# Performance work log

Hardware: AMD Instinct MI355X
Metric: run time of the kernel (lower is better)

## Reference

```python
import jax, jax.numpy as jnp
import numpy as np

B, N, FIN, H, L = 64, 512, 1024, 128, 512
K1, K2, K3 = 256, 128, 64  # top-k pooling keeps half the nodes each stage
CO = 32  # 4 conv branches (k=3,5,7,9) x 32 channels = 128 text-CNN features


def _gcn(A, X, W, b):
    deg = A.sum(-1)
    d = jnp.where(deg > 0, jax.lax.rsqrt(deg), 0.0)
    h = (X @ W) * d[..., None]          # project first (FIN -> H reduces work)
    h = jnp.einsum('bnm,bmh->bnh', A, h)
    return h * d[..., None] + b


def _pool(A, X, p, k):
    # Lupool ~ TopKPooling: learned projection score, keep top-k nodes, gate features
    score = jnp.tanh((X @ p) / (jnp.linalg.norm(p) + 1e-12))  # [B, n]
    _, idx = jax.lax.top_k(score, k)                          # [B, k]
    Xs = jnp.take_along_axis(X, idx[..., None], axis=1)
    Xs = Xs * jnp.take_along_axis(score, idx, axis=1)[..., None]
    As = jax.vmap(lambda a, i: a[i][:, i])(A, idx)            # induced subgraph
    return As, Xs


def _readout(X):
    # DGL AvgPooling / MaxPooling over nodes, concatenated -> [B, 2H]
    return jnp.concatenate([X.mean(axis=1), X.max(axis=1)], axis=1)


def _conv_branch(x_ncl, w, b):
    y = jax.lax.conv_general_dilated(x_ncl, w, (1,), 'VALID',
                                     dimension_numbers=('NCH', 'OIH', 'NCH'))
    return jax.nn.relu(y + b[None, :, None]).max(axis=2)  # global max over time


def setup_inputs():
    key = jax.random.key(0)
    ks = jax.random.split(key, 20)
    u = jax.random.uniform(ks[0], (B, N, N))
    A = (u < 0.01).astype(jnp.float32)
    A = jnp.maximum(A, jnp.swapaxes(A, 1, 2))
    A = A.at[:, jnp.arange(N), jnp.arange(N)].set(1.0)

    def pr(i, shape):
        return jax.random.normal(ks[i], shape, jnp.float32) * 0.05

    return {
        'adj': A,
        'feat': jax.random.normal(ks[1], (B, N, FIN), jnp.float32),
        'pad_dmap': jax.random.normal(ks[2], (B, L, FIN), jnp.float32),
        'W1': pr(3, (FIN, H)), 'b1': jnp.zeros((H,), jnp.float32), 'p1': pr(4, (H,)),
        'W2': pr(5, (H, H)), 'b2': jnp.zeros((H,), jnp.float32), 'p2': pr(6, (H,)),
        'W3': pr(7, (H, H)), 'b3': jnp.zeros((H,), jnp.float32), 'p3': pr(8, (H,)),
        'cat_w': pr(9, (2 * H, H)), 'cat_b': jnp.zeros((H,), jnp.float32),
        'cw0': pr(10, (CO, FIN, 3)), 'cb0': jnp.zeros((CO,), jnp.float32),
        'cw1': pr(11, (CO, FIN, 5)), 'cb1': jnp.zeros((CO,), jnp.float32),
        'cw2': pr(12, (CO, FIN, 7)), 'cb2': jnp.zeros((CO,), jnp.float32),
        'cw3': pr(13, (CO, FIN, 9)), 'cb3': jnp.zeros((CO,), jnp.float32),
        'tf_w': pr(14, (4 * CO, H)), 'tf_b': jnp.zeros((H,), jnp.float32),
        'w1_gate': jnp.array(0.5, jnp.float32),
        'fc1_w': pr(15, (H, 512)), 'fc1_b': jnp.zeros((512,), jnp.float32),
        'fc2_w': pr(16, (512, 256)), 'fc2_b': jnp.zeros((256,), jnp.float32),
        'out_w': pr(17, (256, 2)), 'out_b': jnp.zeros((2,), jnp.float32),
    }


def reference(adj, feat, pad_dmap, W1, b1, p1, W2, b2, p2, W3, b3, p3,
              cat_w, cat_b, cw0, cb0, cw1, cb1, cw2, cb2, cw3, cb3,
              tf_w, tf_b, w1_gate, fc1_w, fc1_b, fc2_w, fc2_b, out_w, out_b):
    # --- 3-stage GraphConv + Lupool with readouts ---
    g1 = jax.nn.relu(_gcn(adj, feat, W1, b1))
    A1, x1 = _pool(adj, g1, p1, K1)
    r1 = _readout(x1)
    g2 = jax.nn.relu(_gcn(A1, x1, W2, b2))
    A2, x2 = _pool(A1, g2, p2, K2)
    r2 = _readout(x2)
    g3 = jax.nn.relu(_gcn(A2, x2, W3, b3))
    A3, x3 = _pool(A2, g3, p3, K3)
    r3 = _readout(x3)
    readout = r1 + r2 + r3                       # [B, 256]
    gnn = jax.nn.relu(readout @ cat_w + cat_b)   # [B, 128]
    # --- text-CNN branch ---
    xt = jnp.swapaxes(pad_dmap, 1, 2)            # [B, FIN, L]
    seq = jnp.concatenate([
        _conv_branch(xt, cw0, cb0), _conv_branch(xt, cw1, cb1),
        _conv_branch(xt, cw2, cb2), _conv_branch(xt, cw3, cb3)], axis=1)  # [B,128]
    seq1 = jax.nn.relu(seq @ tf_w + tf_b)
    # --- gated fusion + MLP head (dropout = identity at inference) ---
    w = jax.nn.sigmoid(w1_gate)
    gc = (1.0 - w) * gnn + w * seq1
    gc = jax.nn.relu(gc @ fc1_w + fc1_b)
    gc = jax.nn.relu(gc @ fc2_w + fc2_b)
    out = jax.nn.relu(gc @ out_w + out_b)
    return jax.nn.softmax(out, axis=1)
```

## Files before the change

kernel.cpp:

```cpp
#include <hip/hip_runtime.h>
#include <math.h>

#define B64  64
#define NN   512
#define FINN 1024
#define HH   128
#define LL   512
#define KK1  256
#define KK2  128
#define KK3  64

typedef __attribute__((ext_vector_type(8))) short short8v;
typedef __attribute__((ext_vector_type(4))) short short4v;
typedef __attribute__((ext_vector_type(4))) float f32x4;

__device__ __forceinline__ float wsum(float v) {
#pragma unroll
    for (int off = 32; off; off >>= 1) v += __shfl_xor(v, off, 64);
    return v;
}

__device__ __forceinline__ short f2bf(float x) {
    union { float f; unsigned u; } v; v.f = x;
    unsigned r = v.u + 0x7fffu + ((v.u >> 16) & 1u);
    return (short)(r >> 16);
}

#define LDAP 40
__global__ __launch_bounds__(256) void mfma_gemm(
    const float* __restrict__ A, const short* __restrict__ BT,
    float* __restrict__ C, int M, int N, int K,
    const float* __restrict__ rowscale, int ntx, int swz)
{
    __shared__ short As[128 * LDAP];
    __shared__ short Bs[128 * LDAP];
    int bid = blockIdx.x;
    if (swz) bid = (bid & 7) * (gridDim.x >> 3) + (bid >> 3);
    const int m0 = (bid / ntx) * 128;
    const int n0 = (bid % ntx) * 128;
    const int tid = threadIdx.x;
    const int lane = tid & 63;
    const int wid = tid >> 6;
    const int wr = (wid >> 1) * 64;
    const int wc = (wid & 1) * 64;

    f32x4 acc[4][4];
#pragma unroll
    for (int i = 0; i < 4; ++i)
#pragma unroll
        for (int j = 0; j < 4; ++j) acc[i][j] = (f32x4){0.f, 0.f, 0.f, 0.f};

    const int srow = tid >> 1;
    const int skq = (tid & 1) * 16;
    const float* Aptr = A + (size_t)(m0 + srow) * K + skq;
    const short* Bptr = BT + (size_t)(n0 + srow) * K + skq;

    const int fr = lane & 15;
    const int fk = (lane >> 4) * 8;
    const int crow = (lane >> 4) * 4;

    for (int k0 = 0; k0 < K; k0 += 32) {
        float4 fa0 = *(const float4*)(Aptr + k0);
        float4 fa1 = *(const float4*)(Aptr + k0 + 4);
        float4 fa2 = *(const float4*)(Aptr + k0 + 8);
        float4 fa3 = *(const float4*)(Aptr + k0 + 12);
        float4 fb0 = *(const float4*)(Bptr + k0);
        float4 fb1 = *(const float4*)(Bptr + k0 + 8);
        __syncthreads();
        short8v ha, hb;
        ha[0] = f2bf(fa0.x); ha[1] = f2bf(fa0.y); ha[2] = f2bf(fa0.z); ha[3] = f2bf(fa0.w);
        ha[4] = f2bf(fa1.x); ha[5] = f2bf(fa1.y); ha[6] = f2bf(fa1.z); ha[7] = f2bf(fa1.w);
        hb[0] = f2bf(fa2.x); hb[1] = f2bf(fa2.y); hb[2] = f2bf(fa2.z); hb[3] = f2bf(fa2.w);
        hb[4] = f2bf(fa3.x); hb[5] = f2bf(fa3.y); hb[6] = f2bf(fa3.z); hb[7] = f2bf(fa3.w);
        *(short8v*)&As[srow * LDAP + skq] = ha;
        *(short8v*)&As[srow * LDAP + skq + 8] = hb;
        *(short8v*)&Bs[srow * LDAP + skq] = *(const short8v*)&fb0;
        *(short8v*)&Bs[srow * LDAP + skq + 8] = *(const short8v*)&fb1;
        __syncthreads();

        short8v af[4], bfr[4];
#pragma unroll
        for (int i = 0; i < 4; ++i) {
            af[i] = *(const short8v*)&As[(wr + i * 16 + fr) * LDAP + fk];
            bfr[i] = *(const short8v*)&Bs[(wc + i * 16 + fr) * LDAP + fk];
        }
#pragma unroll
        for (int mi = 0; mi < 4; ++mi)
#pragma unroll
            for (int ni = 0; ni < 4; ++ni)
                acc[mi][ni] = __builtin_amdgcn_mfma_f32_16x16x32_bf16(
                    af[mi], bfr[ni], acc[mi][ni], 0, 0, 0);
    }

#pragma unroll
    for (int mi = 0; mi < 4; ++mi) {
#pragma unroll
        for (int ni = 0; ni < 4; ++ni) {
            int col = n0 + wc + ni * 16 + fr;
#pragma unroll
            for (int r = 0; r < 4; ++r) {
                int row = m0 + wr + mi * 16 + crow + r;
                float v = acc[mi][ni][r];
                if (rowscale) v *= rowscale[row];
                C[(size_t)row * N + col] = v;
            }
        }
    }
}

__global__ __launch_bounds__(256) void prep_kernel(
    const float* __restrict__ adj, float* __restrict__ dinv,
    const float* __restrict__ cw0, const float* __restrict__ cw1,
    const float* __restrict__ cw2, const float* __restrict__ cw3,
    short* __restrict__ WT,
    const float* __restrict__ W1, short* __restrict__ W1T,
    const float* __restrict__ W2, short* __restrict__ W2T,
    const float* __restrict__ W3, short* __restrict__ W3T,
    const float* __restrict__ p1, const float* __restrict__ p2,
    const float* __restrict__ p3, float* __restrict__ pnorm)
{
    const int bid = blockIdx.x, tid = threadIdx.x;
    if (bid < 8192) {
        int wid = (bid * 256 + tid) >> 6;
        int lane = tid & 63;
        const float* Arow = adj + (size_t)wid * NN;
        float s = 0.f;
        for (int c = lane; c < NN; c += 64) s += Arow[c];
        s = wsum(s);
        if (lane == 0) dinv[wid] = (s > 0.f) ? rsqrtf(s) : 0.f;
    } else if (bid < 8960) {
        int e = (bid - 8192) * 1024 + tid * 4;
        int col = e >> 10, ci = e & 1023;
        const float* cw; int k, base;
        if (col < 96)       { cw = cw0; k = 3; base = 0; }
        else if (col < 256) { cw = cw1; k = 5; base = 96; }
        else if (col < 480) { cw = cw2; k = 7; base = 256; }
        else                { cw = cw3; k = 9; base = 480; }
        int rel = col - base;
        int j = rel >> 5, co = rel & 31;
        short4v o;
#pragma unroll
        for (int q = 0; q < 4; ++q)
            o[q] = f2bf(cw[((size_t)co * FINN + ci + q) * k + j]);
        *(short4v*)&WT[e] = o;
    } else if (bid < 9088) {
        int e = (bid - 8960) * 1024 + tid * 4;
        int n = e >> 10, kq = e & 1023;
        short4v o;
#pragma unroll
        for (int q = 0; q < 4; ++q) o[q] = f2bf(W1[(size_t)(kq + q) * HH + n]);
        *(short4v*)&W1T[e] = o;
    } else if (bid < 9104) {
        int e = (bid - 9088) * 1024 + tid * 4;
        int n = e >> 7, kq = e & 127;
        short4v o;
#pragma unroll
        for (int q = 0; q < 4; ++q) o[q] = f2bf(W2[(size_t)(kq + q) * HH + n]);
        *(short4v*)&W2T[e] = o;
    } else if (bid < 9120) {
        int e = (bid - 9104) * 1024 + tid * 4;
        int n = e >> 7, kq = e & 127;
        short4v o;
#pragma unroll
        for (int q = 0; q < 4; ++q) o[q] = f2bf(W3[(size_t)(kq + q) * HH + n]);
        *(short4v*)&W3T[e] = o;
    } else {
        int w = tid >> 6, lane = tid & 63;
        if (w < 3) {
            const float* p = (w == 0) ? p1 : (w == 1) ? p2 : p3;
            float v0 = p[lane], v1 = p[lane + 64];
            float s = wsum(v0 * v0 + v1 * v1);
            if (lane == 0) pnorm[w] = sqrtf(s);
        }
    }
}

__global__ __launch_bounds__(256) void spmm_gcn(
    const float* __restrict__ A, const float* __restrict__ Hin,
    const float* __restrict__ dinv, const float* __restrict__ bias,
    const float* __restrict__ p, const float* __restrict__ pnorm,
    float* __restrict__ Gout, float* __restrict__ score, int n)
{
    int wid = (blockIdx.x * blockDim.x + threadIdx.x) >> 6;
    int lane = threadIdx.x & 63;
    int b = wid / n, row = wid % n;
    const float* Arow = A + ((size_t)b * n + row) * n;
    float acc0 = 0.f, acc1 = 0.f;
    for (int c = 0; c < n; c += 64) {
        float av = Arow[c + lane];
        unsigned long long mask = __ballot(av != 0.0f);
        while (mask) {
            int i = __ffsll((unsigned long long)mask) - 1;
            mask &= mask - 1;
            float val = __shfl(av, i, 64);
            const float* hr = Hin + ((size_t)b * n + c + i) * HH;
            acc0 = fmaf(val, hr[lane], acc0);
            acc1 = fmaf(val, hr[lane + 64], acc1);
        }
    }
    float dv = dinv[b * n + row];
    float g0 = fmaxf(fmaf(acc0, dv, bias[lane]), 0.f);
    float g1 = fmaxf(fmaf(acc1, dv, bias[lane + 64]), 0.f);
    float* gr = Gout + ((size_t)b * n + row) * HH;
    gr[lane] = g0;
    gr[lane + 64] = g1;
    float s = g0 * p[lane] + g1 * p[lane + 64];
    s = wsum(s);
    if (lane == 0) score[b * n + row] = tanhf(s / (pnorm[0] + 1e-12f));
}

__global__ __launch_bounds__(256) void topk_kernel(
    const float* __restrict__ score, int* __restrict__ idx_out, int n, int k)
{
    __shared__ float sv[512];
    __shared__ int si[512];
    int b = blockIdx.x, tid = threadIdx.x;
    for (int j = tid; j < n; j += blockDim.x) { sv[j] = score[b * n + j]; si[j] = j; }
    __syncthreads();
    for (int sz = 2; sz <= n; sz <<= 1) {
        for (int st = sz >> 1; st; st >>= 1) {
            for (int t = tid; t < (n >> 1); t += blockDim.x) {
                int i = ((t / st) * (st << 1)) + (t % st);
                int j = i + st;
                float vi = sv[i], vj = sv[j];
                int ii = si[i], ij = si[j];
                bool descend = ((i & sz) == 0);
                bool igreater = (vi > vj) || (vi == vj && ii < ij);
                if (igreater != descend) {
                    sv[i] = vj; sv[j] = vi;
                    si[i] = ij; si[j] = ii;
                }
            }
            __syncthreads();
        }
    }
    for (int j = tid; j < k; j += blockDim.x) idx_out[b * k + j] = si[j];
}

__global__ __launch_bounds__(256) void gatherA_kernel(
    const float* __restrict__ Ain, const int* __restrict__ idx,
    float* __restrict__ Aout, float* __restrict__ dinv_out, int n, int k)
{
    int wid = (blockIdx.x * blockDim.x + threadIdx.x) >> 6;
    int lane = threadIdx.x & 63;
    int b = wid / k, i = wid % k;
    int isrc = idx[b * k + i];
    const float* src = Ain + ((size_t)b * n + isrc) * n;
    float s = 0.f;
    for (int c = lane; c < k; c += 64) {
        int jsrc = idx[b * k + c];
        float v = src[jsrc];
        Aout[((size_t)b * k + i) * k + c] = v;
        s += v;
    }
    s = wsum(s);
    if (lane == 0) dinv_out[b * k + i] = rsqrtf(s);
}

__global__ __launch_bounds__(256) void pool_finish(
    const float* __restrict__ G, const float* __restrict__ score,
    const int* __restrict__ idx, float* __restrict__ X, float* __restrict__ R,
    int n, int k, int first, int writex)
{
    __shared__ int lidx[256];
    __shared__ float lsc[256];
    __shared__ float ps[2][128], pm[2][128];
    int b = blockIdx.x, tid = threadIdx.x;
    for (int i = tid; i < k; i += 256) {
        int ii = idx[b * k + i];
        lidx[i] = ii;
        lsc[i] = score[b * n + ii];
    }
    __syncthreads();
    int h = tid & 127, half = tid >> 7;
    int i0 = half * (k >> 1), i1 = i0 + (k >> 1);
    float s = 0.f, m = -INFINITY;
    for (int i = i0; i < i1; ++i) {
        float v = G[((size_t)b * n + lidx[i]) * HH + h] * lsc[i];
        if (writex) X[((size_t)b * k + i) * HH + h] = v;
        s += v;
        m = fmaxf(m, v);
    }
    ps[half][h] = s;
    pm[half][h] = m;
    __syncthreads();
    if (tid < 128) {
        float st = ps[0][h] + ps[1][h];
        float mt = fmaxf(pm[0][h], pm[1][h]);
        float mean = st / (float)k;
        if (first) {
            R[b * 256 + h] = mean;
            R[b * 256 + 128 + h] = mt;
        } else {
            R[b * 256 + h] += mean;
            R[b * 256 + 128 + h] += mt;
        }
    }
}

__global__ __launch_bounds__(256) void conv_reduce(
    const float* __restrict__ P,
    const float* __restrict__ cb0, const float* __restrict__ cb1,
    const float* __restrict__ cb2, const float* __restrict__ cb3,
    float* __restrict__ seq)
{
    int bid = blockIdx.x;
    int chunk = bid & 7, br = (bid >> 3) & 3, b = bid >> 5;
    int k = 3 + 2 * br;
    int base = (br == 0) ? 0 : (br == 1) ? 96 : (br == 2) ? 256 : 480;
    int T = LL - k + 1;
    int co = threadIdx.x & 31, ts = threadIdx.x >> 5;
    const float* cb = (br == 0) ? cb0 : (br == 1) ? cb1 : (br == 2) ? cb2 : cb3;
    float bias = cb[co];
    int c0 = chunk * 64;
    int cend = (c0 + 64 < T) ? c0 + 64 : T;
    float m = -INFINITY;
    for (int t = c0 + ts; t < cend; t += 8) {
        float acc = 0.f;
        for (int j = 0; j < k; ++j)
            acc += P[((size_t)b * LL + t + j) * 768 + base + j * 32 + co];
        m = fmaxf(m, acc + bias);
    }
    __shared__ float red[256];
    red[threadIdx.x] = m;
    __syncthreads();
    if (threadIdx.x < 32) {
        for (int s = 1; s < 8; ++s) m = fmaxf(m, red[co + s * 32]);
        atomicMax((int*)&seq[b * 128 + br * 32 + co], __float_as_int(fmaxf(m, 0.f)));
    }
}

__global__ __launch_bounds__(256) void head_fused(
    const float* __restrict__ seq, const float* __restrict__ tf_w,
    const float* __restrict__ tf_b,
    const float* __restrict__ R, const float* __restrict__ cat_w,
    const float* __restrict__ cat_b,
    const float* __restrict__ w1_gate,
    const float* __restrict__ fc1_w, const float* __restrict__ fc1_b,
    const float* __restrict__ fc2_w, const float* __restrict__ fc2_b,
    const float* __restrict__ out_w, const float* __restrict__ out_b,
    float* __restrict__ out)
{
    int b = blockIdx.x, tid = threadIdx.x;
    __shared__ float sq[128], rr[256], g0[128], g1[512], g2[256];
    rr[tid] = R[b * 256 + tid];
    if (tid < 128) sq[tid] = seq[b * 128 + tid];
    __syncthreads();
    if (tid < 128) {
        float a = tf_b[tid];
        for (int i = 0; i < 128; ++i) a = fmaf(sq[i], tf_w[i * 128 + tid], a);
        float s1 = fmaxf(a, 0.f);
        float c = cat_b[tid];
        for (int i = 0; i < 256; ++i) c = fmaf(rr[i], cat_w[i * 128 + tid], c);
        float gn = fmaxf(c, 0.f);
        float w = 1.f / (1.f + expf(-w1_gate[0]));
        g0[tid] = (1.f - w) * gn + w * s1;
    }
    __syncthreads();
    for (int o = tid; o < 512; o += 256) {
        float a = fc1_b[o];
        for (int i = 0; i < 128; ++i) a = fmaf(g0[i], fc1_w[i * 512 + o], a);
        g1[o] = fmaxf(a, 0.f);
    }
    __syncthreads();
    {
        int o = tid;
        float a = fc2_b[o];
        for (int i = 0; i < 512; ++i) a = fmaf(g1[i], fc2_w[i * 256 + o], a);
        g2[o] = fmaxf(a, 0.f);
    }
    __syncthreads();
    if (tid < 64) {
        float a0 = 0.f, a1 = 0.f;
        for (int q = tid; q < 256; q += 64) {
            a0 = fmaf(g2[q], out_w[q * 2 + 0], a0);
            a1 = fmaf(g2[q], out_w[q * 2 + 1], a1);
        }
        a0 = wsum(a0);
        a1 = wsum(a1);
        if (tid == 0) {
            float l0 = fmaxf(a0 + out_b[0], 0.f);
            float l1 = fmaxf(a1 + out_b[1], 0.f);
            float mm = fmaxf(l0, l1);
            float e0 = expf(l0 - mm), e1 = expf(l1 - mm);
            float d = e0 + e1;
            out[b * 2 + 0] = e0 / d;
            out[b * 2 + 1] = e1 / d;
        }
    }
}

extern "C" void kernel_launch(void* const* d_in, const int* in_sizes, int n_in,
                              void* d_out, int out_size, void* d_ws, size_t ws_size,
                              hipStream_t stream)
{
    const float* adj      = (const float*)d_in[0];
    const float* feat     = (const float*)d_in[1];
    const float* pad_dmap = (const float*)d_in[2];
    const float* W1 = (const float*)d_in[3];
    const float* b1 = (const float*)d_in[4];
    const float* p1 = (const float*)d_in[5];
    const float* W2 = (const float*)d_in[6];
    const float* b2 = (const float*)d_in[7];
    const float* p2 = (const float*)d_in[8];
    const float* W3 = (const float*)d_in[9];
    const float* b3 = (const float*)d_in[10];
    const float* p3 = (const float*)d_in[11];
    const float* cat_w = (const float*)d_in[12];
    const float* cat_b = (const float*)d_in[13];
    const float* cw0 = (const float*)d_in[14];
    const float* cb0 = (const float*)d_in[15];
    const float* cw1 = (const float*)d_in[16];
    const float* cb1 = (const float*)d_in[17];
    const float* cw2 = (const float*)d_in[18];
    const float* cb2 = (const float*)d_in[19];
    const float* cw3 = (const float*)d_in[20];
    const float* cb3 = (const float*)d_in[21];
    const float* tf_w = (const float*)d_in[22];
    const float* tf_b = (const float*)d_in[23];
    const float* w1_gate = (const float*)d_in[24];
    const float* fc1_w = (const float*)d_in[25];
    const float* fc1_b = (const float*)d_in[26];
    const float* fc2_w = (const float*)d_in[27];
    const float* fc2_b = (const float*)d_in[28];
    const float* out_w = (const float*)d_in[29];
    const float* out_b = (const float*)d_in[30];
    float* out = (float*)d_out;

    char* ws = (char*)d_ws;
    auto al = [](size_t x) { return (x + 255) & ~(size_t)255; };
    size_t off = 0;
    auto alloc = [&](size_t nbytes) { size_t o = off; off += al(nbytes); return o; };

    float* pnorm  = (float*)(ws + alloc(3 * 4));
    float* dinv1  = (float*)(ws + alloc((size_t)B64 * NN * 4));
    float* score1 = (float*)(ws + alloc((size_t)B64 * NN * 4));
    int*   idx1   = (int*)  (ws + alloc((size_t)B64 * KK1 * 4));
    float* dinv2  = (float*)(ws + alloc((size_t)B64 * KK1 * 4));
    float* score2 = (float*)(ws + alloc((size_t)B64 * KK1 * 4));
    int*   idx2   = (int*)  (ws + alloc((size_t)B64 * KK2 * 4));
    float* dinv3  = (float*)(ws + alloc((size_t)B64 * KK2 * 4));
    float* score3 = (float*)(ws + alloc((size_t)B64 * KK2 * 4));
    int*   idx3   = (int*)  (ws + alloc((size_t)B64 * KK3 * 4));
    float* R      = (float*)(ws + alloc((size_t)B64 * 256 * 4));
    float* seq    = (float*)(ws + alloc((size_t)B64 * 128 * 4));
    short* W1T    = (short*)(ws + alloc((size_t)HH * FINN * 2));
    short* W2T    = (short*)(ws + alloc((size_t)HH * HH * 2));
    short* W3T    = (short*)(ws + alloc((size_t)HH * HH * 2));

    size_t big = off;
    short* WT = (short*)(ws + big);
    size_t cnnoff = big + al((size_t)768 * FINN * 2);
    float* P = (float*)(ws + cnnoff);
    size_t cnn_end = cnnoff + al((size_t)B64 * LL * 768 * 4);
    size_t g = big;
    float* HT = (float*)(ws + g); g += al((size_t)B64 * NN * HH * 4);
    float* G  = (float*)(ws + g); g += al((size_t)B64 * NN * HH * 4);
    float* A1 = (float*)(ws + g); g += al((size_t)B64 * KK1 * KK1 * 4);
    float* X1 = (float*)(ws + g); g += al((size_t)B64 * KK1 * HH * 4);
    float* A2 = (float*)(ws + g); g += al((size_t)B64 * KK2 * KK2 * 4);
    float* X2 = (float*)(ws + g); g += al((size_t)B64 * KK2 * HH * 4);
    size_t gnn_end = g;
    size_t need = (cnn_end > gnn_end) ? cnn_end : gnn_end;
    if (ws_size < need) return;

    hipMemsetAsync(seq, 0, (size_t)B64 * 128 * 4, stream);

    prep_kernel<<<9121, 256, 0, stream>>>(adj, dinv1, cw0, cw1, cw2, cw3, WT,
                                          W1, W1T, W2, W2T, W3, W3T,
                                          p1, p2, p3, pnorm);

    mfma_gemm<<<1536, 256, 0, stream>>>(pad_dmap, WT, P, B64 * LL, 768, FINN,
                                        nullptr, 6, 1);
    conv_reduce<<<2048, 256, 0, stream>>>(P, cb0, cb1, cb2, cb3, seq);

    mfma_gemm<<<256, 256, 0, stream>>>(feat, W1T, HT, B64 * NN, HH, FINN,
                                       dinv1, 1, 0);
    spmm_gcn<<<(B64 * NN) / 4, 256, 0, stream>>>(adj, HT, dinv1, b1, p1, pnorm + 0,
                                                 G, score1, NN);
    topk_kernel<<<B64, 256, 0, stream>>>(score1, idx1, NN, KK1);
    gatherA_kernel<<<(B64 * KK1) / 4, 256, 0, stream>>>(adj, idx1, A1, dinv2, NN, KK1);
    pool_finish<<<B64, 256, 0, stream>>>(G, score1, idx1, X1, R, NN, KK1, 1, 1);

    mfma_gemm<<<128, 256, 0, stream>>>(X1, W2T, HT, B64 * KK1, HH, HH,
                                       dinv2, 1, 0);
    spmm_gcn<<<(B64 * KK1) / 4, 256, 0, stream>>>(A1, HT, dinv2, b2, p2, pnorm + 1,
                                                  G, score2, KK1);
    topk_kernel<<<B64, 256, 0, stream>>>(score2, idx2, KK1, KK2);
    gatherA_kernel<<<(B64 * KK2) / 4, 256, 0, stream>>>(A1, idx2, A2, dinv3, KK1, KK2);
    pool_finish<<<B64, 256, 0, stream>>>(G, score2, idx2, X2, R, KK1, KK2, 0, 1);

    mfma_gemm<<<64, 256, 0, stream>>>(X2, W3T, HT, B64 * KK2, HH, HH,
                                      dinv3, 1, 0);
    spmm_gcn<<<(B64 * KK2) / 4, 256, 0, stream>>>(A2, HT, dinv3, b3, p3, pnorm + 2,
                                                  G, score3, KK2);
    topk_kernel<<<B64, 256, 0, stream>>>(score3, idx3, KK2, KK3);
    pool_finish<<<B64, 256, 0, stream>>>(G, score3, idx3, nullptr, R, KK2, KK3, 0, 0);

    head_fused<<<B64, 256, 0, stream>>>(seq, tf_w, tf_b, R, cat_w, cat_b, w1_gate,
                                        fc1_w, fc1_b, fc2_w, fc2_b, out_w, out_b,
                                        out);
}
```

Measured before the change: 802.8 us.

## Replace sparse ballot SpMM with dense transposed MFMA GEMMs and fuse score/topk/pool

Computes each GCN stage as two bf16 MFMA GEMMs in a transposed feature-major layout. The first projects features into a bf16 intermediate scaled by dinv. The second multiplies that intermediate by the dense adjacency, using A's symmetry, with a fused dinv/bias/ReLU epilogue. The wave-per-row ballot-based sparse SpMM is removed, trading irregular gathers for dense tensor-core work over a roughly 1%-dense adjacency. Score computation, top-k sort and pooling readout are merged into one per-batch kernel, which drops two launches per stage. This adds bf16 rounding of the intermediate and adjacency, and the score loop reads the transposed G with strided access.

```diff
diff --git a/kernel.cpp b/kernel.cpp
--- a/kernel.cpp
+++ b/kernel.cpp
@@ -27,6 +27,7 @@
 }
 
 #define LDAP 40
+
 __global__ __launch_bounds__(256) void mfma_gemm(
     const float* __restrict__ A, const short* __restrict__ BT,
     float* __restrict__ C, int M, int N, int K,
@@ -103,6 +104,92 @@
                 float v = acc[mi][ni][r];
                 if (rowscale) v *= rowscale[row];
                 C[(size_t)row * N + col] = v;
+            }
+        }
+    }
+}
+
+template <int EPI>
+__global__ __launch_bounds__(256) void tgemm(
+    const short* __restrict__ A, const float* __restrict__ Bt,
+    void* __restrict__ Cout, int K, int npb, int a_per_batch,
+    const float* __restrict__ dinv, const float* __restrict__ bias)
+{
+    __shared__ short As[128 * LDAP];
+    __shared__ short Bs[128 * LDAP];
+    const int n0 = blockIdx.x * 128;
+    const int b = n0 / npb;
+    const int nloc = n0 - b * npb;
+    const int tid = threadIdx.x;
+    const int lane = tid & 63;
+    const int wid = tid >> 6;
+    const int wr = (wid >> 1) * 64;
+    const int wc = (wid & 1) * 64;
+
+    f32x4 acc[4][4];
+#pragma unroll
+    for (int i = 0; i < 4; ++i)
+#pragma unroll
+        for (int j = 0; j < 4; ++j) acc[i][j] = (f32x4){0.f, 0.f, 0.f, 0.f};
+
+    const int srow = tid >> 1;
+    const int skq = (tid & 1) * 16;
+    const short* Aptr = A + (size_t)((a_per_batch ? b * 128 : 0) + srow) * K + skq;
+    const float* Bptr = Bt + (size_t)(n0 + srow) * K + skq;
+
+    const int fr = lane & 15;
+    const int fk = (lane >> 4) * 8;
+    const int crow = (lane >> 4) * 4;
+
+    for (int k0 = 0; k0 < K; k0 += 32) {
+        short8v a0 = *(const short8v*)(Aptr + k0);
+        short8v a1 = *(const short8v*)(Aptr + k0 + 8);
+        float4 fb0 = *(const float4*)(Bptr + k0);
+        float4 fb1 = *(const float4*)(Bptr + k0 + 4);
+        float4 fb2 = *(const float4*)(Bptr + k0 + 8);
+        float4 fb3 = *(const float4*)(Bptr + k0 + 12);
+        __syncthreads();
+        short8v hb0, hb1;
+        hb0[0] = f2bf(fb0.x); hb0[1] = f2bf(fb0.y); hb0[2] = f2bf(fb0.z); hb0[3] = f2bf(fb0.w);
+        hb0[4] = f2bf(fb1.x); hb0[5] = f2bf(fb1.y); hb0[6] = f2bf(fb1.z); hb0[7] = f2bf(fb1.w);
+        hb1[0] = f2bf(fb2.x); hb1[1] = f2bf(fb2.y); hb1[2] = f2bf(fb2.z); hb1[3] = f2bf(fb2.w);
+        hb1[4] = f2bf(fb3.x); hb1[5] = f2bf(fb3.y); hb1[6] = f2bf(fb3.z); hb1[7] = f2bf(fb3.w);
+        *(short8v*)&As[srow * LDAP + skq] = a0;
+        *(short8v*)&As[srow * LDAP + skq + 8] = a1;
+        *(short8v*)&Bs[srow * LDAP + skq] = hb0;
+        *(short8v*)&Bs[srow * LDAP + skq + 8] = hb1;
+        __syncthreads();
+
+        short8v af[4], bfr[4];
+#pragma unroll
+        for (int i = 0; i < 4; ++i) {
+            af[i] = *(const short8v*)&As[(wr + i * 16 + fr) * LDAP + fk];
+            bfr[i] = *(const short8v*)&Bs[(wc + i * 16 + fr) * LDAP + fk];
+        }
+#pragma unroll
+        for (int mi = 0; mi < 4; ++mi)
+#pragma unroll
+            for (int ni = 0; ni < 4; ++ni)
+                acc[mi][ni] = __builtin_amdgcn_mfma_f32_16x16x32_bf16(
+                    af[mi], bfr[ni], acc[mi][ni], 0, 0, 0);
+    }
+
+#pragma unroll
+    for (int mi = 0; mi < 4; ++mi) {
+#pragma unroll
+        for (int ni = 0; ni < 4; ++ni) {
+            int node_t = wc + ni * 16 + fr;
+            float dv = dinv[n0 + node_t];
+#pragma unroll
+            for (int r = 0; r < 4; ++r) {
+                int f = wr + mi * 16 + crow + r;
+                size_t oidx = ((size_t)(b * 128 + f)) * npb + nloc + node_t;
+                float v = acc[mi][ni][r] * dv;
+                if constexpr (EPI == 0) {
+                    ((short*)Cout)[oidx] = f2bf(v);
+                } else {
+                    ((float*)Cout)[oidx] = fmaxf(v + bias[f], 0.f);
+                }
             }
         }
     }
@@ -175,51 +262,32 @@
     }
 }
 
-__global__ __launch_bounds__(256) void spmm_gcn(
-    const float* __restrict__ A, const float* __restrict__ Hin,
-    const float* __restrict__ dinv, const float* __restrict__ bias,
-    const float* __restrict__ p, const float* __restrict__ pnorm,
-    float* __restrict__ Gout, float* __restrict__ score, int n)
-{
-    int wid = (blockIdx.x * blockDim.x + threadIdx.x) >> 6;
-    int lane = threadIdx.x & 63;
-    int b = wid / n, row = wid % n;
-    const float* Arow = A + ((size_t)b * n + row) * n;
-    float acc0 = 0.f, acc1 = 0.f;
-    for (int c = 0; c < n; c += 64) {
-        float av = Arow[c + lane];
-        unsigned long long mask = __ballot(av != 0.0f);
-        while (mask) {
-            int i = __ffsll((unsigned long long)mask) - 1;
-            mask &= mask - 1;
-            float val = __shfl(av, i, 64);
-            const float* hr = Hin + ((size_t)b * n + c + i) * HH;
-            acc0 = fmaf(val, hr[lane], acc0);
-            acc1 = fmaf(val, hr[lane + 64], acc1);
-        }
-    }
-    float dv = dinv[b * n + row];
-    float g0 = fmaxf(fmaf(acc0, dv, bias[lane]), 0.f);
-    float g1 = fmaxf(fmaf(acc1, dv, bias[lane + 64]), 0.f);
-    float* gr = Gout + ((size_t)b * n + row) * HH;
-    gr[lane] = g0;
-    gr[lane + 64] = g1;
-    float s = g0 * p[lane] + g1 * p[lane + 64];
-    s = wsum(s);
-    if (lane == 0) score[b * n + row] = tanhf(s / (pnorm[0] + 1e-12f));
-}
-
-__global__ __launch_bounds__(256) void topk_kernel(
-    const float* __restrict__ score, int* __restrict__ idx_out, int n, int k)
+__global__ __launch_bounds__(256) void score_topk_pool(
+    const float* __restrict__ Gt, const float* __restrict__ p,
+    const float* __restrict__ pnorm, int* __restrict__ idx_out,
+    float* __restrict__ X, float* __restrict__ R,
+    int npb, int k, int first, int writex)
 {
     __shared__ float sv[512];
     __shared__ int si[512];
+    __shared__ float pp[128];
+    __shared__ float ps[2][128], pm[2][128];
     int b = blockIdx.x, tid = threadIdx.x;
-    for (int j = tid; j < n; j += blockDim.x) { sv[j] = score[b * n + j]; si[j] = j; }
-    __syncthreads();
-    for (int sz = 2; sz <= n; sz <<= 1) {
+    if (tid < 128) pp[tid] = p[tid];
+    __syncthreads();
+    const float* Gb = Gt + (size_t)b * 128 * npb;
+    float pn = pnorm[0] + 1e-12f;
+    for (int j = tid; j < npb; j += 256) {
+        float s = 0.f;
+#pragma unroll 4
+        for (int f = 0; f < 128; ++f) s = fmaf(Gb[(size_t)f * npb + j], pp[f], s);
+        sv[j] = tanhf(s / pn);
+        si[j] = j;
+    }
+    __syncthreads();
+    for (int sz = 2; sz <= npb; sz <<= 1) {
         for (int st = sz >> 1; st; st >>= 1) {
-            for (int t = tid; t < (n >> 1); t += blockDim.x) {
+            for (int t = tid; t < (npb >> 1); t += 256) {
                 int i = ((t / st) * (st << 1)) + (t % st);
                 int j = i + st;
                 float vi = sv[i], vj = sv[j];
@@ -234,7 +302,30 @@
             __syncthreads();
         }
     }
-    for (int j = tid; j < k; j += blockDim.x) idx_out[b * k + j] = si[j];
+    for (int j = tid; j < k; j += 256) idx_out[b * k + j] = si[j];
+    int f = tid & 127, iset = tid >> 7;
+    float s = 0.f, m = -INFINITY;
+    for (int i = iset; i < k; i += 2) {
+        float v = Gb[(size_t)f * npb + si[i]] * sv[i];
+        if (writex) X[((size_t)b * k + i) * HH + f] = v;
+        s += v;
+        m = fmaxf(m, v);
+    }
+    ps[iset][f] = s;
+    pm[iset][f] = m;
+    __syncthreads();
+    if (tid < 128) {
+        float st = ps[0][f] + ps[1][f];
+        float mt = fmaxf(pm[0][f], pm[1][f]);
+        float mean = st / (float)k;
+        if (first) {
+            R[b * 256 + f] = mean;
+            R[b * 256 + 128 + f] = mt;
+        } else {
+            R[b * 256 + f] += mean;
+            R[b * 256 + 128 + f] += mt;
+        }
+    }
 }
 
 __global__ __launch_bounds__(256) void gatherA_kernel(
@@ -255,47 +346,6 @@
     }
     s = wsum(s);
     if (lane == 0) dinv_out[b * k + i] = rsqrtf(s);
-}
-
-__global__ __launch_bounds__(256) void pool_finish(
-    const float* __restrict__ G, const float* __restrict__ score,
-    const int* __restrict__ idx, float* __restrict__ X, float* __restrict__ R,
-    int n, int k, int first, int writex)
-{
-    __shared__ int lidx[256];
-    __shared__ float lsc[256];
-    __shared__ float ps[2][128], pm[2][128];
-    int b = blockIdx.x, tid = threadIdx.x;
-    for (int i = tid; i < k; i += 256) {
-        int ii = idx[b * k + i];
-        lidx[i] = ii;
-        lsc[i] = score[b * n + ii];
-    }
-    __syncthreads();
-    int h = tid & 127, half = tid >> 7;
-    int i0 = half * (k >> 1), i1 = i0 + (k >> 1);
-    float s = 0.f, m = -INFINITY;
-    for (int i = i0; i < i1; ++i) {
-        float v = G[((size_t)b * n + lidx[i]) * HH + h] * lsc[i];
-        if (writex) X[((size_t)b * k + i) * HH + h] = v;
-        s += v;
-        m = fmaxf(m, v);
-    }
-    ps[half][h] = s;
-    pm[half][h] = m;
-    __syncthreads();
-    if (tid < 128) {
-        float st = ps[0][h] + ps[1][h];
-        float mt = fmaxf(pm[0][h], pm[1][h]);
-        float mean = st / (float)k;
-        if (first) {
-            R[b * 256 + h] = mean;
-            R[b * 256 + 128 + h] = mt;
-        } else {
-            R[b * 256 + h] += mean;
-            R[b * 256 + 128 + h] += mt;
-        }
-    }
 }
 
 __global__ __launch_bounds__(256) void conv_reduce(
@@ -434,13 +484,10 @@
 
     float* pnorm  = (float*)(ws + alloc(3 * 4));
     float* dinv1  = (float*)(ws + alloc((size_t)B64 * NN * 4));
-    float* score1 = (float*)(ws + alloc((size_t)B64 * NN * 4));
+    float* dinv2  = (float*)(ws + alloc((size_t)B64 * KK1 * 4));
+    float* dinv3  = (float*)(ws + alloc((size_t)B64 * KK2 * 4));
     int*   idx1   = (int*)  (ws + alloc((size_t)B64 * KK1 * 4));
-    float* dinv2  = (float*)(ws + alloc((size_t)B64 * KK1 * 4));
-    float* score2 = (float*)(ws + alloc((size_t)B64 * KK1 * 4));
     int*   idx2   = (int*)  (ws + alloc((size_t)B64 * KK2 * 4));
-    float* dinv3  = (float*)(ws + alloc((size_t)B64 * KK2 * 4));
-    float* score3 = (float*)(ws + alloc((size_t)B64 * KK2 * 4));
     int*   idx3   = (int*)  (ws + alloc((size_t)B64 * KK3 * 4));
     float* R      = (float*)(ws + alloc((size_t)B64 * 256 * 4));
     float* seq    = (float*)(ws + alloc((size_t)B64 * 128 * 4));
@@ -454,12 +501,16 @@
     float* P = (float*)(ws + cnnoff);
     size_t cnn_end = cnnoff + al((size_t)B64 * LL * 768 * 4);
     size_t g = big;
-    float* HT = (float*)(ws + g); g += al((size_t)B64 * NN * HH * 4);
-    float* G  = (float*)(ws + g); g += al((size_t)B64 * NN * HH * 4);
-    float* A1 = (float*)(ws + g); g += al((size_t)B64 * KK1 * KK1 * 4);
-    float* X1 = (float*)(ws + g); g += al((size_t)B64 * KK1 * HH * 4);
-    float* A2 = (float*)(ws + g); g += al((size_t)B64 * KK2 * KK2 * 4);
-    float* X2 = (float*)(ws + g); g += al((size_t)B64 * KK2 * HH * 4);
+    short* Ht1 = (short*)(ws + g); g += al((size_t)B64 * HH * NN * 2);
+    float* Gt1 = (float*)(ws + g); g += al((size_t)B64 * HH * NN * 4);
+    float* A1  = (float*)(ws + g); g += al((size_t)B64 * KK1 * KK1 * 4);
+    float* X1  = (float*)(ws + g); g += al((size_t)B64 * KK1 * HH * 4);
+    short* Ht2 = (short*)(ws + g); g += al((size_t)B64 * HH * KK1 * 2);
+    float* Gt2 = (float*)(ws + g); g += al((size_t)B64 * HH * KK1 * 4);
+    float* A2  = (float*)(ws + g); g += al((size_t)B64 * KK2 * KK2 * 4);
+    float* X2  = (float*)(ws + g); g += al((size_t)B64 * KK2 * HH * 4);
+    short* Ht3 = (short*)(ws + g); g += al((size_t)B64 * HH * KK2 * 2);
+    float* Gt3 = (float*)(ws + g); g += al((size_t)B64 * HH * KK2 * 4);
     size_t gnn_end = g;
     size_t need = (cnn_end > gnn_end) ? cnn_end : gnn_end;
     if (ws_size < need) return;
@@ -474,28 +525,22 @@
                                         nullptr, 6, 1);
     conv_reduce<<<2048, 256, 0, stream>>>(P, cb0, cb1, cb2, cb3, seq);
 
-    mfma_gemm<<<256, 256, 0, stream>>>(feat, W1T, HT, B64 * NN, HH, FINN,
-                                       dinv1, 1, 0);
-    spmm_gcn<<<(B64 * NN) / 4, 256, 0, stream>>>(adj, HT, dinv1, b1, p1, pnorm + 0,
-                                                 G, score1, NN);
-    topk_kernel<<<B64, 256, 0, stream>>>(score1, idx1, NN, KK1);
+    tgemm<0><<<256, 256, 0, stream>>>(W1T, feat, Ht1, FINN, NN, 0, dinv1, nullptr);
+    tgemm<1><<<256, 256, 0, stream>>>(Ht1, adj, Gt1, NN, NN, 1, dinv1, b1);
+    score_topk_pool<<<B64, 256, 0, stream>>>(Gt1, p1, pnorm + 0, idx1, X1, R,
+                                             NN, KK1, 1, 1);
     gatherA_kernel<<<(B64 * KK1) / 4, 256, 0, stream>>>(adj, idx1, A1, dinv2, NN, KK1);
-    pool_finish<<<B64, 256, 0, stream>>>(G, score1, idx1, X1, R, NN, KK1, 1, 1);
-
-    mfma_gemm<<<128, 256, 0, stream>>>(X1, W2T, HT, B64 * KK1, HH, HH,
-                                       dinv2, 1, 0);
-    spmm_gcn<<<(B64 * KK1) / 4, 256, 0, stream>>>(A1, HT, dinv2, b2, p2, pnorm + 1,
-                                                  G, score2, KK1);
-    topk_kernel<<<B64, 256, 0, stream>>>(score2, idx2, KK1, KK2);
+
+    tgemm<0><<<128, 256, 0, stream>>>(W2T, X1, Ht2, HH, KK1, 0, dinv2, nullptr);
+    tgemm<1><<<128, 256, 0, stream>>>(Ht2, A1, Gt2, KK1, KK1, 1, dinv2, b2);
+    score_topk_pool<<<B64, 256, 0, stream>>>(Gt2, p2, pnorm + 1, idx2, X2, R,
+                                             KK1, KK2, 0, 1);
     gatherA_kernel<<<(B64 * KK2) / 4, 256, 0, stream>>>(A1, idx2, A2, dinv3, KK1, KK2);
-    pool_finish<<<B64, 256, 0, stream>>>(G, score2, idx2, X2, R, KK1, KK2, 0, 1);
-
-    mfma_gemm<<<64, 256, 0, stream>>>(X2, W3T, HT, B64 * KK2, HH, HH,
-                                      dinv3, 1, 0);
-    spmm_gcn<<<(B64 * KK2) / 4, 256, 0, stream>>>(A2, HT, dinv3, b3, p3, pnorm + 2,
-                                                  G, score3, KK2);
-    topk_kernel<<<B64, 256, 0, stream>>>(score3, idx3, KK2, KK3);
-    pool_finish<<<B64, 256, 0, stream>>>(G, score3, idx3, nullptr, R, KK2, KK3, 0, 0);
+
+    tgemm<0><<<64, 256, 0, stream>>>(W3T, X2, Ht3, HH, KK2, 0, dinv3, nullptr);
+    tgemm<1><<<64, 256, 0, stream>>>(Ht3, A2, Gt3, KK2, KK2, 1, dinv3, b3);
+    score_topk_pool<<<B64, 256, 0, stream>>>(Gt3, p3, pnorm + 2, idx3, nullptr, R,
+                                             KK2, KK3, 0, 0);
 
     head_fused<<<B64, 256, 0, stream>>>(seq, tf_w, tf_b, R, cat_w, cat_b, w1_gate,
                                         fc1_w, fc1_b, fc2_w, fc2_b, out_w, out_b,
```

Result: faster. 755.7 us (-5.9%).
